# Kernel optimization log

Measured on AMD Instinct MI355X. Metric: run time of the kernel, lower is better.

## Reference

```python
import jax, jax.numpy as jnp
import numpy as np

TEMPERATURE = 0.1
GAMMA = 0.5
LOSS_WEIGHT = 1.0
LINE_CLASS = 2
COS_EPS = 1e-8      # torch F.cosine_similarity eps
RADIUS = 1.0        # positive-pair spatial radius
SELF_EPS = 1e-6     # excludes self pairs (dist ~ 0) from positives
NCE_EPS = 1e-6


def _pairwise_dist(coords):
    # Euclidean cdist [N, N] with a sqrt that is safe at 0 (self pairs)
    sq = jnp.sum(coords * coords, axis=1)
    d2 = jnp.maximum(sq[:, None] + sq[None, :] - 2.0 * (coords @ coords.T), 0.0)
    safe = jnp.where(d2 > 0.0, d2, 1.0)
    return jnp.where(d2 > 0.0, jnp.sqrt(safe), 0.0)


def setup_inputs() -> dict:
    key = jax.random.key(0)
    k1, k2, k3 = jax.random.split(key, 3)
    N, D = 4096, 64
    features = jax.random.normal(k1, (N, D), dtype=jnp.float32)
    # uniform in a 10x10x10 box -> ~30 neighbors within radius 1.0 per point
    coords = jax.random.uniform(k2, (N, 3), dtype=jnp.float32) * 10.0
    labels = jax.random.randint(k3, (N,), 0, 3)  # class 2 == power line
    return {"features": features, "labels": labels, "coords": coords}


def reference(features, labels, coords):
    # Static-shape equivalent of boolean-indexing the line-class points:
    # weight w_i = 1 iff labels[i] == LINE_CLASS. All sums / means below are
    # restricted to line points via w, matching torch masked gather exactly.
    w = (labels == LINE_CLASS).astype(features.dtype)        # [N]
    M = jnp.sum(w)                                           # number of line points
    pair_w = w[:, None] * w[None, :]                         # [N, N]

    # cosine similarity matrix  [N, N]
    norms = jnp.maximum(jnp.linalg.norm(features, axis=1, keepdims=True), COS_EPS)
    fn = features / norms
    feat_sim = fn @ fn.T

    # spatial distance matrix and pos / neg pair masks  [N, N]
    coord_dist = _pairwise_dist(coords)
    pos_raw = ((coord_dist < RADIUS) & (coord_dist > SELF_EPS)).astype(features.dtype)
    pos_w = pair_w * pos_raw
    neg_w = pair_w * (1.0 - pos_raw)   # ~pos_mask within line subset (incl. self)

    # InfoNCE over line points
    exp_sim = jnp.exp(feat_sim / TEMPERATURE)
    pos_sum = jnp.sum(exp_sim * pos_w, axis=1)               # [N]
    neg_sum = jnp.sum(exp_sim * neg_w, axis=1)               # [N]
    ratio = pos_sum / (neg_sum + pos_sum + NCE_EPS)
    per_point = -jnp.log(jnp.where(w > 0, ratio, 1.0))       # 0 for non-line pts
    info_nce = jnp.sum(per_point) / M                        # mean over line pts

    # continuity: mean over the M x M line-pair block
    feat_dist = 1.0 - feat_sim
    continuity = jnp.sum(jnp.abs(feat_dist - coord_dist) * pos_w) / (M * M)

    return (info_nce + GAMMA * continuity) * LOSS_WEIGHT
```

## Files before the change

### kernel.cpp

```cpp
#include <hip/hip_runtime.h>
#include <hip/hip_bf16.h>

#define LINE_CLASS 2
#define NJ 32
#define MAXCHUNK 128

__global__ __launch_bounds__(256) void pair_kernel(const float* __restrict__ feat,
                                                   const int* __restrict__ labels,
                                                   const float* __restrict__ coords,
                                                   int N,
                                                   int* __restrict__ Mout,
                                                   float* __restrict__ posp,
                                                   float* __restrict__ negp,
                                                   float* __restrict__ contp) {
    const int b   = blockIdx.x;
    const int js  = blockIdx.y;
    const int tid = threadIdx.x;
    const int r   = tid & 63;
    const int q   = tid >> 6;

    __shared__ int    scnt[256];
    __shared__ int    ownIdx[64];
    __shared__ int    jIdx[MAXCHUNK];
    __shared__ float4 jcC[MAXCHUNK];
    __shared__ float  fj[MAXCHUNK * 64];
    __shared__ float  sp[4][64], sn[4][64], sc[256];

    const int EPT = (N + 255) / 256;
    const int i0  = tid * EPT;
    unsigned long long bits = 0ull;
    for (int u = 0; u < EPT; ++u) {
        const int i = i0 + u;
        if (i < N && labels[i] == LINE_CLASS) bits |= (1ull << u);
    }
    const int cnt = __popcll(bits);
    scnt[tid] = cnt;
    __syncthreads();
    for (int s = 1; s < 256; s <<= 1) {
        int v = scnt[tid];
        if (tid >= s) v += scnt[tid - s];
        __syncthreads();
        scnt[tid] = v;
        __syncthreads();
    }
    const int M = scnt[255];
    if (b == 0 && js == 0 && tid == 0) *Mout = M;

    const int own0 = b * 64;
    if (own0 >= M) return;

    int chunk = (M + NJ - 1) / NJ;
    if (chunk > MAXCHUNK) chunk = MAXCHUNK;
    const int j0   = js * chunk;
    const int j1   = (j0 + chunk < M) ? (j0 + chunk) : M;
    const int jcnt = j1 - j0;
    const int k    = own0 + r;

    if (jcnt <= 0) {
        if (q == 0) {
            posp[(size_t)js * N + k] = 0.0f;
            negp[(size_t)js * N + k] = 0.0f;
        }
        if (tid == 0) contp[b * NJ + js] = 0.0f;
        return;
    }

    int pos = scnt[tid] - cnt;
    for (int u = 0; u < EPT; ++u) {
        if (bits & (1ull << u)) {
            const int i  = i0 + u;
            const int dO = pos - own0;
            if (dO >= 0 && dO < 64) ownIdx[dO] = i;
            const int dJ = pos - j0;
            if (dJ >= 0 && dJ < jcnt) jIdx[dJ] = i;
            ++pos;
        }
    }
    __syncthreads();

    for (int t = tid; t < jcnt; t += 256) {
        const int i = jIdx[t];
        const float x = coords[i * 3 + 0];
        const float y = coords[i * 3 + 1];
        const float z = coords[i * 3 + 2];
        jcC[t] = make_float4(x, y, z, fmaf(x, x, fmaf(y, y, z * z)));
    }
    for (int jj = q; jj < jcnt; jj += 4) {
        const int i = jIdx[jj];
        const float v = feat[(size_t)i * 64 + r];
        float ss = v * v;
        #pragma unroll
        for (int off = 32; off > 0; off >>= 1) ss += __shfl_xor(ss, off);
        const float inv = 1.0f / fmaxf(sqrtf(ss), 1e-8f);
        fj[jj * 64 + r] = v * inv;
    }

    const bool valid = (k < M);
    float4 f4[16];
    float4 ci;
    if (valid) {
        const int i = ownIdx[r];
        const float4* fr = (const float4*)(feat + (size_t)i * 64);
        float ss = 0.0f;
        #pragma unroll
        for (int t = 0; t < 16; ++t) {
            f4[t] = fr[t];
            ss = fmaf(f4[t].x, f4[t].x, ss);
            ss = fmaf(f4[t].y, f4[t].y, ss);
            ss = fmaf(f4[t].z, f4[t].z, ss);
            ss = fmaf(f4[t].w, f4[t].w, ss);
        }
        const float inv = 1.0f / fmaxf(sqrtf(ss), 1e-8f);
        #pragma unroll
        for (int t = 0; t < 16; ++t) {
            f4[t].x *= inv; f4[t].y *= inv; f4[t].z *= inv; f4[t].w *= inv;
        }
        const float x = coords[i * 3 + 0];
        const float y = coords[i * 3 + 1];
        const float z = coords[i * 3 + 2];
        ci = make_float4(x, y, z, fmaf(x, x, fmaf(y, y, z * z)));
    } else {
        #pragma unroll
        for (int t = 0; t < 16; ++t) f4[t] = make_float4(0.f, 0.f, 0.f, 0.f);
        ci = make_float4(0.f, 0.f, 0.f, 0.f);
    }
    __syncthreads();

    float pos_s = 0.0f, neg_s = 0.0f, cont_s = 0.0f;
    for (int jj = q; jj < jcnt; jj += 4) {
        const float4* __restrict__ fv = (const float4*)(fj + jj * 64);
        float dot = 0.0f;
        #pragma unroll
        for (int t = 0; t < 16; ++t) {
            const float4 bv = fv[t];
            dot = fmaf(f4[t].x, bv.x, dot);
            dot = fmaf(f4[t].y, bv.y, dot);
            dot = fmaf(f4[t].z, bv.z, dot);
            dot = fmaf(f4[t].w, bv.w, dot);
        }
        const float4 cj = jcC[jj];
        const float cdot = fmaf(ci.x, cj.x, fmaf(ci.y, cj.y, ci.z * cj.z));
        const float d2 = fmaxf(ci.w + cj.w - 2.0f * cdot, 0.0f);
        const float dist = (d2 > 0.0f) ? sqrtf(d2) : 0.0f;
        const float e = expf(dot * 10.0f);
        const bool isPos = (dist < 1.0f) && (dist > 1e-6f);
        if (isPos) {
            pos_s += e;
            if (valid) cont_s += fabsf((1.0f - dot) - dist);
        } else {
            neg_s += e;
        }
    }

    sp[q][r] = pos_s;
    sn[q][r] = neg_s;
    sc[tid]  = cont_s;
    __syncthreads();
    if (q == 0) {
        posp[(size_t)js * N + k] = sp[0][r] + sp[1][r] + sp[2][r] + sp[3][r];
        negp[(size_t)js * N + k] = sn[0][r] + sn[1][r] + sn[2][r] + sn[3][r];
    }
    for (int s = 128; s > 0; s >>= 1) {
        if (tid < s) sc[tid] += sc[tid + s];
        __syncthreads();
    }
    if (tid == 0) contp[b * NJ + js] = sc[0];
}

__global__ __launch_bounds__(1024) void final_kernel(const float* __restrict__ posp,
                                                     const float* __restrict__ negp,
                                                     const float* __restrict__ contp,
                                                     const int* __restrict__ Mp,
                                                     int N,
                                                     float* __restrict__ out) {
    const int tid = threadIdx.x;
    const int M = *Mp;
    float nce = 0.0f;
    for (int k = tid; k < M; k += 1024) {
        float P = 0.0f, Ng = 0.0f;
        #pragma unroll
        for (int js = 0; js < NJ; ++js) {
            P  += posp[(size_t)js * N + k];
            Ng += negp[(size_t)js * N + k];
        }
        const float ratio = fmaxf(P / (Ng + P + 1e-6f), 1e-38f);
        nce += -logf(ratio);
    }
    float cont = 0.0f;
    const int nact = (M + 63) / 64;
    const int nslots = nact * NJ;
    for (int c = tid; c < nslots; c += 1024) cont += contp[c];

    __shared__ float r1[1024];
    __shared__ float r2[1024];
    r1[tid] = nce;
    r2[tid] = cont;
    __syncthreads();
    for (int s = 512; s > 0; s >>= 1) {
        if (tid < s) { r1[tid] += r1[tid + s]; r2[tid] += r2[tid + s]; }
        __syncthreads();
    }
    if (tid == 0) {
        const float Mf = (float)M;
        out[0] = (r1[0] / Mf + 0.5f * (r2[0] / (Mf * Mf))) * 1.0f;
    }
}

extern "C" void kernel_launch(void* const* d_in, const int* in_sizes, int n_in,
                              void* d_out, int out_size, void* d_ws, size_t ws_size,
                              hipStream_t stream) {
    const float* feat   = (const float*)d_in[0];
    const int*   labels = (const int*)  d_in[1];
    const float* coords = (const float*)d_in[2];
    const int N = in_sizes[1];

    char* ws = (char*)d_ws;
    int*   Mp    = (int*)  (ws + 0);
    float* posp  = (float*)(ws + 1024);
    float* negp  = (float*)(ws + 1024 + (size_t)4 * NJ * N);
    float* contp = (float*)(ws + 1024 + (size_t)8 * NJ * N);

    const int NB = (N + 63) / 64;

    pair_kernel<<<dim3(NB, NJ), 256, 0, stream>>>(feat, labels, coords, N,
                                                  Mp, posp, negp, contp);
    final_kernel<<<1, 1024, 0, stream>>>(posp, negp, contp, Mp, N, (float*)d_out);
}
```

Before: 108.1 us.

## Move label compaction and feature normalization into a separate prep kernel

Adds a prep kernel that does the line-point compaction (index list and count) once and writes normalized features and coords-plus-squared-norm for every point into the workspace. The pair kernel no longer repeats the prefix scan and normalization in each of its blocks. It now reads j-features straight from global memory with a wave-uniform index instead of staging them in shared memory. This removes redundant per-block scans and normalization, at the cost of an extra launch and more scattered global/L2 reads in the inner loop.

```diff
diff --git a/kernel.cpp b/kernel.cpp
--- a/kernel.cpp
+++ b/kernel.cpp
@@ -3,13 +3,66 @@
 
 #define LINE_CLASS 2
 #define NJ 32
-#define MAXCHUNK 128
-
-__global__ __launch_bounds__(256) void pair_kernel(const float* __restrict__ feat,
+
+__global__ __launch_bounds__(256) void prep_kernel(const float* __restrict__ feat,
                                                    const int* __restrict__ labels,
                                                    const float* __restrict__ coords,
                                                    int N,
-                                                   int* __restrict__ Mout,
+                                                   int* __restrict__ idx,
+                                                   int* __restrict__ Mp,
+                                                   float* __restrict__ fnAll,
+                                                   float4* __restrict__ cAll) {
+    const int tid = threadIdx.x;
+
+    if (blockIdx.x == 0) {
+        __shared__ int scnt[256];
+        const int EPT = (N + 255) / 256;
+        const int i0  = tid * EPT;
+        unsigned long long bits = 0ull;
+        for (int u = 0; u < EPT; ++u) {
+            const int i = i0 + u;
+            if (i < N && labels[i] == LINE_CLASS) bits |= (1ull << u);
+        }
+        const int cnt = __popcll(bits);
+        scnt[tid] = cnt;
+        __syncthreads();
+        for (int s = 1; s < 256; s <<= 1) {
+            int v = scnt[tid];
+            if (tid >= s) v += scnt[tid - s];
+            __syncthreads();
+            scnt[tid] = v;
+            __syncthreads();
+        }
+        int pos = scnt[tid] - cnt;
+        for (int u = 0; u < EPT; ++u) {
+            if (bits & (1ull << u)) idx[pos++] = i0 + u;
+        }
+        if (tid == 255) *Mp = scnt[255];
+        return;
+    }
+
+    const int i = (blockIdx.x - 1) * 4 + (tid >> 6);
+    const int d = tid & 63;
+    if (i >= N) return;
+    const float v = feat[(size_t)i * 64 + d];
+    float ss = v * v;
+    #pragma unroll
+    for (int off = 32; off > 0; off >>= 1) ss += __shfl_xor(ss, off);
+    const float dn = fmaxf(sqrtf(ss), 1e-8f);
+    fnAll[(size_t)i * 64 + d] = v / dn;
+    if (d == 0) {
+        const float x = coords[i * 3 + 0];
+        const float y = coords[i * 3 + 1];
+        const float z = coords[i * 3 + 2];
+        cAll[i] = make_float4(x, y, z, fmaf(x, x, fmaf(y, y, z * z)));
+    }
+}
+
+__global__ __launch_bounds__(256) void pair_kernel(const float* __restrict__ fnAll,
+                                                   const float4* __restrict__ cAll,
+                                                   const int* __restrict__ idx,
+                                                   const int* __restrict__ Mp,
+                                                   int N,
                                                    float* __restrict__ posp,
                                                    float* __restrict__ negp,
                                                    float* __restrict__ contp) {
@@ -18,46 +71,22 @@
     const int tid = threadIdx.x;
     const int r   = tid & 63;
     const int q   = tid >> 6;
-
-    __shared__ int    scnt[256];
-    __shared__ int    ownIdx[64];
-    __shared__ int    jIdx[MAXCHUNK];
-    __shared__ float4 jcC[MAXCHUNK];
-    __shared__ float  fj[MAXCHUNK * 64];
-    __shared__ float  sp[4][64], sn[4][64], sc[256];
-
-    const int EPT = (N + 255) / 256;
-    const int i0  = tid * EPT;
-    unsigned long long bits = 0ull;
-    for (int u = 0; u < EPT; ++u) {
-        const int i = i0 + u;
-        if (i < N && labels[i] == LINE_CLASS) bits |= (1ull << u);
-    }
-    const int cnt = __popcll(bits);
-    scnt[tid] = cnt;
-    __syncthreads();
-    for (int s = 1; s < 256; s <<= 1) {
-        int v = scnt[tid];
-        if (tid >= s) v += scnt[tid - s];
-        __syncthreads();
-        scnt[tid] = v;
-        __syncthreads();
-    }
-    const int M = scnt[255];
-    if (b == 0 && js == 0 && tid == 0) *Mout = M;
-
+    const int M   = *Mp;
     const int own0 = b * 64;
+    const int k    = own0 + r;
+
     if (own0 >= M) return;
-
-    int chunk = (M + NJ - 1) / NJ;
-    if (chunk > MAXCHUNK) chunk = MAXCHUNK;
+    const bool valid = (k < M);
+
+    const int chunk = (M + NJ - 1) / NJ;
     const int j0   = js * chunk;
     const int j1   = (j0 + chunk < M) ? (j0 + chunk) : M;
     const int jcnt = j1 - j0;
-    const int k    = own0 + r;
+
+    __shared__ float sp[4][64], sn[4][64], sc[256];
 
     if (jcnt <= 0) {
-        if (q == 0) {
+        if (q == 0 && valid) {
             posp[(size_t)js * N + k] = 0.0f;
             negp[(size_t)js * N + k] = 0.0f;
         }
@@ -65,80 +94,35 @@
         return;
     }
 
-    int pos = scnt[tid] - cnt;
-    for (int u = 0; u < EPT; ++u) {
-        if (bits & (1ull << u)) {
-            const int i  = i0 + u;
-            const int dO = pos - own0;
-            if (dO >= 0 && dO < 64) ownIdx[dO] = i;
-            const int dJ = pos - j0;
-            if (dJ >= 0 && dJ < jcnt) jIdx[dJ] = i;
-            ++pos;
-        }
-    }
-    __syncthreads();
-
-    for (int t = tid; t < jcnt; t += 256) {
-        const int i = jIdx[t];
-        const float x = coords[i * 3 + 0];
-        const float y = coords[i * 3 + 1];
-        const float z = coords[i * 3 + 2];
-        jcC[t] = make_float4(x, y, z, fmaf(x, x, fmaf(y, y, z * z)));
-    }
-    for (int jj = q; jj < jcnt; jj += 4) {
-        const int i = jIdx[jj];
-        const float v = feat[(size_t)i * 64 + r];
-        float ss = v * v;
-        #pragma unroll
-        for (int off = 32; off > 0; off >>= 1) ss += __shfl_xor(ss, off);
-        const float inv = 1.0f / fmaxf(sqrtf(ss), 1e-8f);
-        fj[jj * 64 + r] = v * inv;
-    }
-
-    const bool valid = (k < M);
     float4 f4[16];
     float4 ci;
     if (valid) {
-        const int i = ownIdx[r];
-        const float4* fr = (const float4*)(feat + (size_t)i * 64);
-        float ss = 0.0f;
-        #pragma unroll
-        for (int t = 0; t < 16; ++t) {
-            f4[t] = fr[t];
-            ss = fmaf(f4[t].x, f4[t].x, ss);
-            ss = fmaf(f4[t].y, f4[t].y, ss);
-            ss = fmaf(f4[t].z, f4[t].z, ss);
-            ss = fmaf(f4[t].w, f4[t].w, ss);
-        }
-        const float inv = 1.0f / fmaxf(sqrtf(ss), 1e-8f);
-        #pragma unroll
-        for (int t = 0; t < 16; ++t) {
-            f4[t].x *= inv; f4[t].y *= inv; f4[t].z *= inv; f4[t].w *= inv;
-        }
-        const float x = coords[i * 3 + 0];
-        const float y = coords[i * 3 + 1];
-        const float z = coords[i * 3 + 2];
-        ci = make_float4(x, y, z, fmaf(x, x, fmaf(y, y, z * z)));
+        const int i = idx[k];
+        const float4* fr = (const float4*)(fnAll + (size_t)i * 64);
+        #pragma unroll
+        for (int t = 0; t < 16; ++t) f4[t] = fr[t];
+        ci = cAll[i];
     } else {
         #pragma unroll
         for (int t = 0; t < 16; ++t) f4[t] = make_float4(0.f, 0.f, 0.f, 0.f);
         ci = make_float4(0.f, 0.f, 0.f, 0.f);
     }
-    __syncthreads();
 
     float pos_s = 0.0f, neg_s = 0.0f, cont_s = 0.0f;
-    for (int jj = q; jj < jcnt; jj += 4) {
-        const float4* __restrict__ fv = (const float4*)(fj + jj * 64);
+    for (int j = j0 + q; j < j1; j += 4) {
+        const int ju = __builtin_amdgcn_readfirstlane(j);
+        const int ij = idx[ju];
+        const float4* __restrict__ fjv = (const float4*)(fnAll + (size_t)ij * 64);
         float dot = 0.0f;
         #pragma unroll
         for (int t = 0; t < 16; ++t) {
-            const float4 bv = fv[t];
+            const float4 bv = fjv[t];
             dot = fmaf(f4[t].x, bv.x, dot);
             dot = fmaf(f4[t].y, bv.y, dot);
             dot = fmaf(f4[t].z, bv.z, dot);
             dot = fmaf(f4[t].w, bv.w, dot);
         }
-        const float4 cj = jcC[jj];
+        const float4 cj = cAll[ij];
         const float cdot = fmaf(ci.x, cj.x, fmaf(ci.y, cj.y, ci.z * cj.z));
         const float d2 = fmaxf(ci.w + cj.w - 2.0f * cdot, 0.0f);
         const float dist = (d2 > 0.0f) ? sqrtf(d2) : 0.0f;
@@ -156,7 +140,7 @@
     sn[q][r] = neg_s;
     sc[tid]  = cont_s;
     __syncthreads();
-    if (q == 0) {
+    if (q == 0 && valid) {
         posp[(size_t)js * N + k] = sp[0][r] + sp[1][r] + sp[2][r] + sp[3][r];
         negp[(size_t)js * N + k] = sn[0][r] + sn[1][r] + sn[2][r] + sn[3][r];
     }
@@ -215,14 +199,19 @@
     const int N = in_sizes[1];
 
     char* ws = (char*)d_ws;
-    int*   Mp    = (int*)  (ws + 0);
-    float* posp  = (float*)(ws + 1024);
-    float* negp  = (float*)(ws + 1024 + (size_t)4 * NJ * N);
-    float* contp = (float*)(ws + 1024 + (size_t)8 * NJ * N);
+    int*    Mp    = (int*)   (ws + 0);
+    int*    idx   = (int*)   (ws + 1024);
+    float4* cAll  = (float4*)(ws + 32768);
+    float*  fnAll = (float*) (ws + 131072);
+    float*  posp  = (float*) (ws + 2097152);
+    float*  negp  = (float*) (ws + 2621440);
+    float*  contp = (float*) (ws + 3145728);
 
     const int NB = (N + 63) / 64;
 
-    pair_kernel<<<dim3(NB, NJ), 256, 0, stream>>>(feat, labels, coords, N,
-                                                  Mp, posp, negp, contp);
+    prep_kernel<<<1 + (N + 3) / 4, 256, 0, stream>>>(feat, labels, coords, N,
+                                                     idx, Mp, fnAll, cAll);
+    pair_kernel<<<dim3(NB, NJ), 256, 0, stream>>>(fnAll, cAll, idx, Mp, N,
+                                                  posp, negp, contp);
     final_kernel<<<1, 1024, 0, stream>>>(posp, negp, contp, Mp, N, (float*)d_out);
 }
```

Result: faster. 88.36 us (median of 2 runs) (-18.3%).

## Read j-features from global memory, use wave-shuffle scan, recount M in final kernel

Applied to the files above, without the earlier changes.

The 256-step shared-memory scan of line counts becomes a wave-level shuffle scan plus a four-entry cross-wave combine. The per-block 32KB LDS tile of normalized j-features is dropped: the inner loop reads raw features straight from global memory (relying on cache hits) and scales by a per-row inverse norm kept in shared memory. The final kernel now counts M itself instead of reading it from workspace. This cuts LDS footprint and barrier count, which could raise occupancy, at the cost of many more global/L2 loads in the hot dot-product loop.

```diff
diff --git a/kernel.cpp b/kernel.cpp
--- a/kernel.cpp
+++ b/kernel.cpp
@@ -5,25 +5,24 @@
 #define NJ 32
 #define MAXCHUNK 128
 
-__global__ __launch_bounds__(256) void pair_kernel(const float* __restrict__ feat,
-                                                   const int* __restrict__ labels,
-                                                   const float* __restrict__ coords,
-                                                   int N,
-                                                   int* __restrict__ Mout,
-                                                   float* __restrict__ posp,
-                                                   float* __restrict__ negp,
-                                                   float* __restrict__ contp) {
+__global__ __launch_bounds__(256) void pair_fused(const float* __restrict__ feat,
+                                                  const int* __restrict__ labels,
+                                                  const float* __restrict__ coords,
+                                                  int N,
+                                                  float* __restrict__ posp,
+                                                  float* __restrict__ negp,
+                                                  float* __restrict__ contp) {
     const int b   = blockIdx.x;
     const int js  = blockIdx.y;
     const int tid = threadIdx.x;
     const int r   = tid & 63;
     const int q   = tid >> 6;
 
-    __shared__ int    scnt[256];
-    __shared__ int    ownIdx[64];
-    __shared__ int    jIdx[MAXCHUNK];
-    __shared__ float4 jcC[MAXCHUNK];
-    __shared__ float  fj[MAXCHUNK * 64];
+    __shared__ int    wtot[4];
+    __shared__ int    sOwn[64];
+    __shared__ int    sJ[MAXCHUNK];
+    __shared__ float  sInv[MAXCHUNK];
+    __shared__ float4 sJC[MAXCHUNK];
     __shared__ float  sp[4][64], sn[4][64], sc[256];
 
     const int EPT = (N + 255) / 256;
@@ -34,17 +33,19 @@
         if (i < N && labels[i] == LINE_CLASS) bits |= (1ull << u);
     }
     const int cnt = __popcll(bits);
-    scnt[tid] = cnt;
-    __syncthreads();
-    for (int s = 1; s < 256; s <<= 1) {
-        int v = scnt[tid];
-        if (tid >= s) v += scnt[tid - s];
-        __syncthreads();
-        scnt[tid] = v;
-        __syncthreads();
-    }
-    const int M = scnt[255];
-    if (b == 0 && js == 0 && tid == 0) *Mout = M;
+    int incl = cnt;
+    #pragma unroll
+    for (int off = 1; off < 64; off <<= 1) {
+        const int t = __shfl_up(incl, off);
+        if (r >= off) incl += t;
+    }
+    if (r == 63) wtot[q] = incl;
+    __syncthreads();
+    int waveBase = 0;
+    #pragma unroll
+    for (int w = 0; w < 4; ++w) waveBase += (w < q) ? wtot[w] : 0;
+    const int M     = wtot[0] + wtot[1] + wtot[2] + wtot[3];
+    const int rank0 = waveBase + incl - cnt;
 
     const int own0 = b * 64;
     if (own0 >= M) return;
@@ -55,9 +56,10 @@
     const int j1   = (j0 + chunk < M) ? (j0 + chunk) : M;
     const int jcnt = j1 - j0;
     const int k    = own0 + r;
+    const bool valid = (k < M);
 
     if (jcnt <= 0) {
-        if (q == 0) {
+        if (q == 0 && valid) {
             posp[(size_t)js * N + k] = 0.0f;
             negp[(size_t)js * N + k] = 0.0f;
         }
@@ -65,41 +67,40 @@
         return;
     }
 
-    int pos = scnt[tid] - cnt;
-    for (int u = 0; u < EPT; ++u) {
-        if (bits & (1ull << u)) {
-            const int i  = i0 + u;
-            const int dO = pos - own0;
-            if (dO >= 0 && dO < 64) ownIdx[dO] = i;
-            const int dJ = pos - j0;
-            if (dJ >= 0 && dJ < jcnt) jIdx[dJ] = i;
-            ++pos;
-        }
-    }
-    __syncthreads();
-
-    for (int t = tid; t < jcnt; t += 256) {
-        const int i = jIdx[t];
-        const float x = coords[i * 3 + 0];
-        const float y = coords[i * 3 + 1];
-        const float z = coords[i * 3 + 2];
-        jcC[t] = make_float4(x, y, z, fmaf(x, x, fmaf(y, y, z * z)));
-    }
+    {
+        int rk = rank0;
+        for (int u = 0; u < EPT; ++u) {
+            if (bits & (1ull << u)) {
+                const int i  = i0 + u;
+                const int dO = rk - own0;
+                if (dO >= 0 && dO < 64) sOwn[dO] = i;
+                const int dJ = rk - j0;
+                if (dJ >= 0 && dJ < jcnt) sJ[dJ] = i;
+                ++rk;
+            }
+        }
+    }
+    __syncthreads();
+
     for (int jj = q; jj < jcnt; jj += 4) {
-        const int i = jIdx[jj];
+        const int i = sJ[jj];
         const float v = feat[(size_t)i * 64 + r];
         float ss = v * v;
         #pragma unroll
         for (int off = 32; off > 0; off >>= 1) ss += __shfl_xor(ss, off);
-        const float inv = 1.0f / fmaxf(sqrtf(ss), 1e-8f);
-        fj[jj * 64 + r] = v * inv;
-    }
-
-    const bool valid = (k < M);
+        if (r == 0) {
+            sInv[jj] = 1.0f / fmaxf(sqrtf(ss), 1e-8f);
+            const float x = coords[i * 3 + 0];
+            const float y = coords[i * 3 + 1];
+            const float z = coords[i * 3 + 2];
+            sJC[jj] = make_float4(x, y, z, fmaf(x, x, fmaf(y, y, z * z)));
+        }
+    }
+
     float4 f4[16];
     float4 ci;
     if (valid) {
-        const int i = ownIdx[r];
+        const int i = sOwn[r];
         const float4* fr = (const float4*)(feat + (size_t)i * 64);
         float ss = 0.0f;
         #pragma unroll
@@ -128,25 +129,28 @@
 
     float pos_s = 0.0f, neg_s = 0.0f, cont_s = 0.0f;
     for (int jj = q; jj < jcnt; jj += 4) {
-        const float4* __restrict__ fv = (const float4*)(fj + jj * 64);
+        const int   ij   = sJ[jj];
+        const float invj = sInv[jj];
+        const float4* __restrict__ fjv = (const float4*)(feat + (size_t)ij * 64);
         float dot = 0.0f;
         #pragma unroll
         for (int t = 0; t < 16; ++t) {
-            const float4 bv = fv[t];
+            const float4 bv = fjv[t];
             dot = fmaf(f4[t].x, bv.x, dot);
             dot = fmaf(f4[t].y, bv.y, dot);
             dot = fmaf(f4[t].z, bv.z, dot);
             dot = fmaf(f4[t].w, bv.w, dot);
         }
-        const float4 cj = jcC[jj];
+        const float sim = dot * invj;
+        const float4 cj = sJC[jj];
         const float cdot = fmaf(ci.x, cj.x, fmaf(ci.y, cj.y, ci.z * cj.z));
         const float d2 = fmaxf(ci.w + cj.w - 2.0f * cdot, 0.0f);
         const float dist = (d2 > 0.0f) ? sqrtf(d2) : 0.0f;
-        const float e = expf(dot * 10.0f);
+        const float e = expf(sim * 10.0f);
         const bool isPos = (dist < 1.0f) && (dist > 1e-6f);
         if (isPos) {
             pos_s += e;
-            if (valid) cont_s += fabsf((1.0f - dot) - dist);
+            if (valid) cont_s += fabsf((1.0f - sim) - dist);
         } else {
             neg_s += e;
         }
@@ -156,7 +160,7 @@
     sn[q][r] = neg_s;
     sc[tid]  = cont_s;
     __syncthreads();
-    if (q == 0) {
+    if (q == 0 && valid) {
         posp[(size_t)js * N + k] = sp[0][r] + sp[1][r] + sp[2][r] + sp[3][r];
         negp[(size_t)js * N + k] = sn[0][r] + sn[1][r] + sn[2][r] + sn[3][r];
     }
@@ -167,14 +171,25 @@
     if (tid == 0) contp[b * NJ + js] = sc[0];
 }
 
-__global__ __launch_bounds__(1024) void final_kernel(const float* __restrict__ posp,
+__global__ __launch_bounds__(1024) void final_kernel(const int* __restrict__ labels,
+                                                     const float* __restrict__ posp,
                                                      const float* __restrict__ negp,
                                                      const float* __restrict__ contp,
-                                                     const int* __restrict__ Mp,
                                                      int N,
                                                      float* __restrict__ out) {
     const int tid = threadIdx.x;
-    const int M = *Mp;
+
+    int c = 0;
+    for (int i = tid; i < N; i += 1024) c += (labels[i] == LINE_CLASS) ? 1 : 0;
+    #pragma unroll
+    for (int off = 32; off > 0; off >>= 1) c += __shfl_xor(c, off);
+    __shared__ int wcnt[16];
+    if ((tid & 63) == 0) wcnt[tid >> 6] = c;
+    __syncthreads();
+    int M = 0;
+    #pragma unroll
+    for (int w = 0; w < 16; ++w) M += wcnt[w];
+
     float nce = 0.0f;
     for (int k = tid; k < M; k += 1024) {
         float P = 0.0f, Ng = 0.0f;
@@ -189,7 +204,7 @@
     float cont = 0.0f;
     const int nact = (M + 63) / 64;
     const int nslots = nact * NJ;
-    for (int c = tid; c < nslots; c += 1024) cont += contp[c];
+    for (int cix = tid; cix < nslots; cix += 1024) cont += contp[cix];
 
     __shared__ float r1[1024];
     __shared__ float r2[1024];
@@ -215,14 +230,14 @@
     const int N = in_sizes[1];
 
     char* ws = (char*)d_ws;
-    int*   Mp    = (int*)  (ws + 0);
-    float* posp  = (float*)(ws + 1024);
-    float* negp  = (float*)(ws + 1024 + (size_t)4 * NJ * N);
-    float* contp = (float*)(ws + 1024 + (size_t)8 * NJ * N);
+    float* posp  = (float*)(ws + 0);
+    float* negp  = (float*)(ws + (size_t)4 * NJ * N);
+    float* contp = (float*)(ws + (size_t)8 * NJ * N);
 
     const int NB = (N + 63) / 64;
 
-    pair_kernel<<<dim3(NB, NJ), 256, 0, stream>>>(feat, labels, coords, N,
-                                                  Mp, posp, negp, contp);
-    final_kernel<<<1, 1024, 0, stream>>>(posp, negp, contp, Mp, N, (float*)d_out);
+    pair_fused<<<dim3(NB, NJ), 256, 0, stream>>>(feat, labels, coords, N,
+                                                 posp, negp, contp);
+    final_kernel<<<1, 1024, 0, stream>>>(labels, posp, negp, contp, N,
+                                         (float*)d_out);
 }
```

After: 128.3 us. 18.7% more time.
